# Optimization experiments

Measured on AMD Instinct MI355X. Metric: run time of the kernel, lower is better.

## Reference

```python
import jax, jax.numpy as jnp
import numpy as np

N_HEADS, N_LEVELS, N_POINTS, D_MODEL = 8, 3, 12, 64
PARAM_NAMES = ['vp0_w','vp0_b','vp1_w','vp1_b','so0_w','so0_b','so1_w','so1_b','so2_w','so2_b','so3_w','so3_b','aw0_w','aw0_b','aw1_w','aw1_b','aw2_w','aw2_b','aw3_w','aw3_b','op0_w','op0_b','op1_w','op1_b']

def _lrelu(x):
    return jnp.where(x >= 0, x, 0.1 * x)

def _conv(x, w, b):
    y = jax.lax.conv_general_dilated(x, w, (1, 1), 'SAME', dimension_numbers=('NCHW', 'OIHW', 'NCHW'))
    return y + b[None, :, None, None]

def _bilinear(img, px, py):
    # img [B,C,H,W]; px,py [B,Q] absolute pixel coords; zero padding (grid_sample 'zeros')
    B, C, H, W = img.shape
    flat = img.reshape(B, C, H * W)
    x0 = jnp.floor(px); y0 = jnp.floor(py)
    wx1 = px - x0; wy1 = py - y0
    def g(xi, yi, wgt):
        valid = (xi >= 0) & (xi <= W - 1) & (yi >= 0) & (yi <= H - 1)
        xi_c = jnp.clip(xi, 0, W - 1).astype(jnp.int32)
        yi_c = jnp.clip(yi, 0, H - 1).astype(jnp.int32)
        v = jnp.take_along_axis(flat, (yi_c * W + xi_c)[:, None, :], axis=2)
        return v * (wgt * valid)[:, None, :]
    return (g(x0, y0, (1 - wx1) * (1 - wy1)) + g(x0 + 1, y0, wx1 * (1 - wy1))
          + g(x0, y0 + 1, (1 - wx1) * wy1) + g(x0 + 1, y0 + 1, wx1 * wy1))

def _flow_warp(img, flow):
    # img [n,C,h,w]; flow [n,2,h,w] (x,y); matches grid_sample align_corners=True
    n, C, h, w = img.shape
    gy, gx = jnp.meshgrid(jnp.arange(h, dtype=img.dtype), jnp.arange(w, dtype=img.dtype), indexing='ij')
    px = (gx[None] + flow[:, 0]).reshape(n, h * w)
    py = (gy[None] + flow[:, 1]).reshape(n, h * w)
    return _bilinear(img, px, py).reshape(n, C, h, w)

def _forward(x, flow_1, flow_2, flip_flow_1, flip_flow_2, p):
    n, t, c, h, w = x.shape
    hw = h * w; THW = t * hw
    M, L, P, D = N_HEADS, N_LEVELS, N_POINTS, c // N_HEADS
    flow_cn1 = flow_1
    flow_cn2 = flow_1 + _flow_warp(flow_2, flow_1)
    flow_n1c, flow_n1n2 = flip_flow_1, flow_2
    flow_n2n1 = flip_flow_2
    flow_n2c = flip_flow_2 + _flow_warp(flip_flow_1, flip_flow_2)
    warp_cn1 = _flow_warp(x[:, 1], flow_cn1)
    warp_cn2 = _flow_warp(x[:, 2], flow_cn2)
    warp_n1c = _flow_warp(x[:, 0], flow_n1c)
    warp_n1n2 = _flow_warp(x[:, 2], flow_n1n2)
    warp_n2n1 = _flow_warp(x[:, 1], flow_n2n1)
    warp_n2c = _flow_warp(x[:, 0], flow_n2c)
    extra = jnp.concatenate([x[:, 0], warp_cn1, warp_cn2, warp_n1c, warp_n1n2, warp_n2n1, warp_n2c,
                             flow_cn1, flow_cn2, flow_n1c, flow_n1n2, flow_n2n1, flow_n2c], axis=1)
    value = _conv(_lrelu(_conv(x.reshape(n, t * c, h, w), p['vp0_w'], p['vp0_b'])), p['vp1_w'], p['vp1_b'])
    def head(e, pre):
        y = _lrelu(_conv(e, p[pre + '0_w'], p[pre + '0_b']))
        y = _lrelu(_conv(y, p[pre + '1_w'], p[pre + '1_b']))
        y = _lrelu(_conv(y, p[pre + '2_w'], p[pre + '2_b']))
        return _conv(y, p[pre + '3_w'], p[pre + '3_b'])
    so = head(extra, 'so')  # [n, L*M*L*P*2, h, w]
    aw = head(extra, 'aw')  # [n, L*M*L*P*9, h, w]
    so = so.reshape(n, t, -1, hw).transpose(0, 1, 3, 2).reshape(n, THW, M, L, P, 2)
    aw = aw.reshape(n, t, -1, hw).transpose(0, 1, 3, 2).reshape(n, THW, M, L * P * 9)
    aw = jax.nn.softmax(aw, axis=-1).reshape(n, THW, M, L, P * 9)
    # flow-guided offsets: add per-(query-frame, target-level) flow to learned offsets
    off = so.reshape(n, t, hw, M, L, P, 2)
    fz = jnp.zeros_like(flow_cn2)
    def lvl(f0, f1, f2):
        s = jnp.stack([f0, f1, f2], 1)  # [n,3,2,h,w]
        return s.transpose(0, 3, 4, 1, 2).reshape(n, hw, L, 2)[:, None, :, None, :, None, :]
    off = jnp.concatenate([
        off[:, 0:1] + lvl(fz, flow_cn1, flow_cn2),
        off[:, 1:2] + lvl(flow_n1c, fz, flow_n1n2),
        off[:, 2:3] + lvl(flow_n2c, flow_n2n1, fz)], axis=1).reshape(n, THW, M, L, P, 2)
    # 3x3 integer patch around each sampling point
    pi, pj = jnp.meshgrid(jnp.arange(-1, 2), jnp.arange(-1, 2), indexing='ij')
    patch = jnp.stack([pi, pj], -1).reshape(1, 1, 1, 1, 1, 9, 2).astype(off.dtype)
    off = (off[..., None, :] + patch).reshape(n, THW, M, L, P * 9, 2)
    # reference points (valid_ratios are all 1: full masks are zeros)
    ry, rx = jnp.meshgrid((jnp.arange(h) + 0.5) / h, (jnp.arange(w) + 0.5) / w, indexing='ij')
    ref = jnp.stack([rx, ry], -1).reshape(1, hw, 2).astype(off.dtype)
    ref = jnp.tile(ref, (1, t, 1))  # [1, THW, 2]
    norm = jnp.array([w, h], dtype=off.dtype)
    loc = ref[:, :, None, None, None, :] + off / norm  # [n,THW,M,L,P*9,2] normalized
    # multi-scale deformable attention (all L levels share (h,w)); align_corners=False, zeros pad
    P9 = P * 9
    v = value.reshape(n, t, c, hw).transpose(0, 1, 3, 2).reshape(n, THW, M, D)
    vl = v.reshape(n, L, hw, M, D).transpose(0, 3, 1, 4, 2).reshape(n * M * L, D, h, w)
    px = (loc[..., 0] * w - 0.5).transpose(0, 2, 3, 1, 4).reshape(n * M * L, THW * P9)
    py = (loc[..., 1] * h - 0.5).transpose(0, 2, 3, 1, 4).reshape(n * M * L, THW * P9)
    sampled = _bilinear(vl, px, py).reshape(n, M, L, D, THW, P9)
    out = jnp.einsum('nmldqp,nqmlp->nqmd', sampled, aw).reshape(n, THW, c)
    out = out.reshape(n, t, h, w, c).transpose(0, 1, 4, 2, 3).reshape(n, t * c, h, w)
    out = _conv(_lrelu(_conv(out, p['op0_w'], p['op0_b'])), p['op1_w'], p['op1_b'])
    return out.reshape(n, t, c, h, w) + x

def setup_inputs():
    key = jax.random.key(0)
    n, t, c, h, w = 1, 3, 64, 32, 32
    ks = jax.random.split(key, 24)
    d = {}
    d['x'] = jax.random.normal(ks[0], (n, t, c, h, w), jnp.float32)
    for i, name in enumerate(['flow_1', 'flow_2', 'flip_flow_1', 'flip_flow_2']):
        d[name] = jax.random.normal(ks[1 + i], (n, 2, h, w), jnp.float32)
    cin_extra = 7 * c + 12
    specs = [('vp0', t * c, t * c), ('vp1', t * c, t * c),
             ('so0', c, cin_extra), ('so1', c, c), ('so2', c, c), ('so3', N_LEVELS * N_HEADS * N_LEVELS * N_POINTS * 2, c),
             ('aw0', c, cin_extra), ('aw1', c, c), ('aw2', c, c), ('aw3', N_LEVELS * N_HEADS * N_LEVELS * N_POINTS * 9, c),
             ('op0', t * c, t * c), ('op1', t * c, t * c)]
    for i, (name, co, ci) in enumerate(specs):
        kw, kb = jax.random.split(ks[5 + i])
        std = (2.0 / (ci * 9)) ** 0.5
        d[name + '_w'] = jax.random.normal(kw, (co, ci, 3, 3), jnp.float32) * std
        d[name + '_b'] = jax.random.normal(kb, (co,), jnp.float32) * 0.01
    return d

def reference(x, flow_1, flow_2, flip_flow_1, flip_flow_2, vp0_w, vp0_b, vp1_w, vp1_b, so0_w, so0_b, so1_w, so1_b, so2_w, so2_b, so3_w, so3_b, aw0_w, aw0_b, aw1_w, aw1_b, aw2_w, aw2_b, aw3_w, aw3_b, op0_w, op0_b, op1_w, op1_b):
    p = dict(zip(PARAM_NAMES, (vp0_w, vp0_b, vp1_w, vp1_b, so0_w, so0_b, so1_w, so1_b, so2_w, so2_b, so3_w, so3_b, aw0_w, aw0_b, aw1_w, aw1_b, aw2_w, aw2_b, aw3_w, aw3_b, op0_w, op0_b, op1_w, op1_b)))
    return _forward(x, flow_1, flow_2, flip_flow_1, flip_flow_2, p)
```

## Files before the change

### kernel.cpp

```cpp
#include <hip/hip_runtime.h>
#include <math.h>

#define HW 1024

typedef __attribute__((ext_vector_type(8))) short bf16x8;
typedef __attribute__((ext_vector_type(4))) float floatx4;

__device__ __forceinline__ unsigned short f2bf(float f) {
    unsigned u = __float_as_uint(f);
    u += 0x7FFF + ((u >> 16) & 1);
    return (unsigned short)(u >> 16);
}
__device__ __forceinline__ float bf2f(unsigned short u) {
    return __uint_as_float(((unsigned)u) << 16);
}
__device__ __forceinline__ float bflo(unsigned u) { return __uint_as_float(u << 16); }
__device__ __forceinline__ float bfhi(unsigned u) { return __uint_as_float(u & 0xffff0000u); }

__device__ __forceinline__ float bilin32(const float* __restrict__ img, float px, float py) {
    float x0f = floorf(px), y0f = floorf(py);
    float wx = px - x0f, wy = py - y0f;
    bool vx0 = (x0f >= 0.f) && (x0f <= 31.f);
    bool vx1 = (x0f >= -1.f) && (x0f <= 30.f);
    bool vy0 = (y0f >= 0.f) && (y0f <= 31.f);
    bool vy1 = (y0f >= -1.f) && (y0f <= 30.f);
    int ix0 = (int)fminf(fmaxf(x0f, 0.f), 31.f);
    int iy0 = (int)fminf(fmaxf(y0f, 0.f), 31.f);
    int ix1 = (int)fminf(fmaxf(x0f + 1.f, 0.f), 31.f);
    int iy1 = (int)fminf(fmaxf(y0f + 1.f, 0.f), 31.f);
    float w00 = (1.f - wx) * (1.f - wy) * ((vx0 && vy0) ? 1.f : 0.f);
    float w01 = wx * (1.f - wy) * ((vx1 && vy0) ? 1.f : 0.f);
    float w10 = (1.f - wx) * wy * ((vx0 && vy1) ? 1.f : 0.f);
    float w11 = wx * wy * ((vx1 && vy1) ? 1.f : 0.f);
    return w00 * img[iy0 * 32 + ix0] + w01 * img[iy0 * 32 + ix1] +
           w10 * img[iy1 * 32 + ix0] + w11 * img[iy1 * 32 + ix1];
}

__device__ __forceinline__ float2 comp_flow(const float* __restrict__ fa,
                                            const float* __restrict__ fb, int pix) {
    int y = pix >> 5, x = pix & 31;
    float fx = fa[pix], fy = fa[HW + pix];
    float px = (float)x + fx, py = (float)y + fy;
    float2 r;
    r.x = fx + bilin32(fb, px, py);
    r.y = fy + bilin32(fb + HW, px, py);
    return r;
}

struct WD { const float* src; int cout, Cin, nCb, wbase, beg; };
struct PrepP {
    const float *x, *f1, *f2, *ff1, *ff2;
    float *fcn2, *fn2c;
    unsigned short *x_pad, *extra_pad, *wgt;
    WD wd[12];
};

__global__ __launch_bounds__(256) void prep_k(PrepP P) {
    __shared__ float wlds[16 * 288];
    const int b = blockIdx.x, tid = threadIdx.x;
    if (b < 192) {
        int idx = b * 256 + tid;
        int pix = idx / 48, c4 = idx - pix * 48;
        int y = pix >> 5, xx = pix & 31;
        int c0 = c4 * 4;
        ushort4 s;
        s.x = f2bf(P.x[(size_t)(c0 + 0) * HW + pix]);
        s.y = f2bf(P.x[(size_t)(c0 + 1) * HW + pix]);
        s.z = f2bf(P.x[(size_t)(c0 + 2) * HW + pix]);
        s.w = f2bf(P.x[(size_t)(c0 + 3) * HW + pix]);
        *(ushort4*)(&P.x_pad[(size_t)((y + 1) * 34 + xx + 1) * 192 + c0]) = s;
    } else if (b < 672) {
        int idx = (b - 192) * 256 + tid;
        int pix = idx / 120, c4 = idx - pix * 120;
        int y = pix >> 5, xx = pix & 31;
        int c0 = c4 * 4;
        float va[4];
        if (c0 < 64) {
#pragma unroll
            for (int k = 0; k < 4; ++k) va[k] = P.x[(size_t)(c0 + k) * HW + pix];
        } else if (c0 < 448) {
            int grp = (c0 - 64) >> 6;
            int c = (c0 - 64) & 63;
            const float* src; float fx, fy;
            if (grp == 0)      { src = P.x + 64 * HW;  fx = P.f1[pix];  fy = P.f1[HW + pix]; }
            else if (grp == 1) { src = P.x + 128 * HW; float2 r = comp_flow(P.f1, P.f2, pix);  fx = r.x; fy = r.y; }
            else if (grp == 2) { src = P.x;            fx = P.ff1[pix]; fy = P.ff1[HW + pix]; }
            else if (grp == 3) { src = P.x + 128 * HW; fx = P.f2[pix];  fy = P.f2[HW + pix]; }
            else if (grp == 4) { src = P.x + 64 * HW;  fx = P.ff2[pix]; fy = P.ff2[HW + pix]; }
            else               { src = P.x;            float2 r = comp_flow(P.ff2, P.ff1, pix); fx = r.x; fy = r.y; }
            float px = (float)xx + fx, py = (float)y + fy;
            float x0f = floorf(px), y0f = floorf(py);
            float wx = px - x0f, wy = py - y0f;
            bool vx0 = (x0f >= 0.f) && (x0f <= 31.f);
            bool vx1 = (x0f >= -1.f) && (x0f <= 30.f);
            bool vy0 = (y0f >= 0.f) && (y0f <= 31.f);
            bool vy1 = (y0f >= -1.f) && (y0f <= 30.f);
            int ix0 = (int)fminf(fmaxf(x0f, 0.f), 31.f);
            int iy0 = (int)fminf(fmaxf(y0f, 0.f), 31.f);
            int ix1 = (int)fminf(fmaxf(x0f + 1.f, 0.f), 31.f);
            int iy1 = (int)fminf(fmaxf(y0f + 1.f, 0.f), 31.f);
            float w00 = (1.f - wx) * (1.f - wy) * ((vx0 && vy0) ? 1.f : 0.f);
            float w01 = wx * (1.f - wy) * ((vx1 && vy0) ? 1.f : 0.f);
            float w10 = (1.f - wx) * wy * ((vx0 && vy1) ? 1.f : 0.f);
            float w11 = wx * wy * ((vx1 && vy1) ? 1.f : 0.f);
            int p00 = iy0 * 32 + ix0, p01 = iy0 * 32 + ix1;
            int p10 = iy1 * 32 + ix0, p11 = iy1 * 32 + ix1;
            const float* im = src + (size_t)c * HW;
#pragma unroll
            for (int k = 0; k < 4; ++k) {
                va[k] = w00 * im[p00] + w01 * im[p01] + w10 * im[p10] + w11 * im[p11];
                im += HW;
            }
        } else {
#pragma unroll
            for (int k = 0; k < 4; ++k) {
                int ch = c0 + k;
                float v = 0.f;
                if (ch < 460) {
                    int fc = ch - 448;
                    int which = fc >> 1, comp = fc & 1;
                    if (which == 0)      v = P.f1[comp * HW + pix];
                    else if (which == 1) { float2 r = comp_flow(P.f1, P.f2, pix);  v = comp ? r.y : r.x; }
                    else if (which == 2) v = P.ff1[comp * HW + pix];
                    else if (which == 3) v = P.f2[comp * HW + pix];
                    else if (which == 4) v = P.ff2[comp * HW + pix];
                    else                 { float2 r = comp_flow(P.ff2, P.ff1, pix); v = comp ? r.y : r.x; }
                }
                va[k] = v;
            }
        }
        ushort4 s;
        s.x = f2bf(va[0]); s.y = f2bf(va[1]); s.z = f2bf(va[2]); s.w = f2bf(va[3]);
        *(ushort4*)(&P.extra_pad[(size_t)((y + 1) * 34 + xx + 1) * 480 + c0]) = s;
    } else if (b < 688) {
        int idx = (b - 672) * 256 + tid;
        if (idx < 1024) {
            float2 r = comp_flow(P.f1, P.f2, idx);
            P.fcn2[idx] = r.x; P.fcn2[HW + idx] = r.y;
        } else if (idx < 2048) {
            int pix = idx - 1024;
            float2 r = comp_flow(P.ff2, P.ff1, pix);
            P.fn2c[pix] = r.x; P.fn2c[HW + pix] = r.y;
        }
    } else if (b < 704) {
        const int chans[9] = {192, 192, 480, 64, 64, 64, 64, 192, 192};
        size_t offs[9]; size_t a = 0;
        for (int i = 0; i < 9; ++i) { offs[i] = a; a += (size_t)1156 * chans[i]; }
        int bb = b - 688;
        for (int item = bb; item < 9 * 132; item += 16) {
            int buf = item / 132, i = item - buf * 132;
            int py, px;
            if (i < 34) { py = 0; px = i; }
            else if (i < 68) { py = 33; px = i - 34; }
            else { int j = i - 68; py = 1 + (j >> 1); px = (j & 1) ? 33 : 0; }
            int C = chans[buf];
            unsigned short* p = P.x_pad + offs[buf] + (size_t)(py * 34 + px) * C;
            for (int c = tid; c < C; c += 256) p[c] = 0;
        }
    } else {
        int blk = b - 704;
        int di = 0;
        while (di < 11 && blk >= P.wd[di + 1].beg) ++di;
        WD w = P.wd[di];
        int local = blk - w.beg;
        int co16 = local / w.nCb, cb = local - co16 * w.nCb;
        int cr0 = co16 * 16, ci0 = cb * 32;
        for (int i = tid; i < 16 * 288; i += 256) {
            int cr = i / 288, o = i - cr * 288;
            int crg = cr0 + cr, ci = ci0 + o / 9;
            float v = (crg < w.cout && ci < w.Cin)
                ? w.src[((size_t)crg * w.Cin + ci0) * 9 + o] : 0.f;
            wlds[i] = v;
        }
        __syncthreads();
        for (int e = tid; e < 9 * 512; e += 256) {
            int t = e >> 9, idx = e & 511;
            int j = idx & 7, lane = idx >> 3, q = lane >> 4, mm = lane & 15;
            P.wgt[((size_t)w.wbase + ((size_t)co16 * 9 + t) * w.nCb + cb) * 512 + idx] =
                f2bf(wlds[mm * 288 + (q * 8 + j) * 9 + t]);
        }
    }
}

struct CDesc {
    const unsigned short* in;
    const unsigned short* wgt;
    const float* bias;
    void* out;
    const float* residual;
    int Cpad, nCb, Cout, mode, cmod, relu, Mblocks;
};
struct CParam { CDesc d[4]; };

template<int PIXROWS, int COBLK>
__global__ __launch_bounds__(256) void conv_mfma_k(CParam P) {
    constexpr int TROWS = PIXROWS + 2;
    constexpr int TC = TROWS * 34 * 4;
    constexpr int ITRIPS = (TC + 255) / 256;
    constexpr int NTY = PIXROWS / 4;
    constexpr int NACC = NTY * 2;
    constexpr int MT = COBLK / 16;
    constexpr int WN = MT * 9 * 64;
    constexpr int WTRIPS = (WN + 255) / 256;
    __shared__ unsigned short blds[TROWS * 34 * 40];
    __shared__ unsigned short wlds[MT * 9 * 512];

    int bx = blockIdx.x;
    int di = 0;
    while (bx >= P.d[di].Mblocks) { bx -= P.d[di].Mblocks; ++di; }
    const CDesc d = P.d[di];

    const int tid = threadIdx.x;
    const int w = tid >> 6, lane = tid & 63;
    const int lq = lane >> 4, ln = lane & 15;
    const int co0 = bx * COBLK;
    const int by = blockIdx.y, y0 = by * PIXROWS;
    const unsigned short* __restrict__ in = d.in;
    const unsigned short* __restrict__ wg = d.wgt;
    const int Cpad = d.Cpad, nCb = d.nCb;

    floatx4 acc[MT][NACC];
#pragma unroll
    for (int mt = 0; mt < MT; ++mt)
#pragma unroll
        for (int nt = 0; nt < NACC; ++nt)
            acc[mt][nt] = (floatx4){0.f, 0.f, 0.f, 0.f};

    bf16x8 ireg[ITRIPS];
    bf16x8 wreg[WTRIPS];

    auto load_regs = [&](int cb) {
        const int ci0 = cb << 5;
#pragma unroll
        for (int k = 0; k < ITRIPS; ++k) {
            int i = tid + k * 256;
            if (i < TC) {
                int r = i / 136, rem = i - r * 136, c = rem >> 2, g = rem & 3;
                ireg[k] = *(const bf16x8*)(in + (size_t)((y0 + r) * 34 + c) * Cpad + ci0 + g * 8);
            }
        }
#pragma unroll
        for (int k = 0; k < WTRIPS; ++k) {
            int i = tid + k * 256;
            if (i < WN) {
                int chunk = i >> 6, l16 = i & 63;
                int mt = chunk / 9, t = chunk - mt * 9;
                wreg[k] = *(const bf16x8*)(wg + ((size_t)(((co0 >> 4) + mt) * 9 + t) * nCb + cb) * 512 + l16 * 8);
            }
        }
    };

    load_regs(0);

    for (int cb = 0; cb < nCb; ++cb) {
        __syncthreads();
#pragma unroll
        for (int k = 0; k < ITRIPS; ++k) {
            int i = tid + k * 256;
            if (i < TC) {
                int r = i / 136, rem = i - r * 136, c = rem >> 2, g = rem & 3;
                *(bf16x8*)(&blds[(r * 34 + c) * 40 + g * 8]) = ireg[k];
            }
        }
#pragma unroll
        for (int k = 0; k < WTRIPS; ++k) {
            int i = tid + k * 256;
            if (i < WN) {
                int chunk = i >> 6, l16 = i & 63;
                *(bf16x8*)(&wlds[chunk * 512 + l16 * 8]) = wreg[k];
            }
        }
        __syncthreads();
        if (cb + 1 < nCb) load_regs(cb + 1);
        for (int t = 0; t < 9; ++t) {
            const int dy = t / 3, dx = t - dy * 3;
            bf16x8 bfr[NACC];
#pragma unroll
            for (int ty = 0; ty < NTY; ++ty)
#pragma unroll
                for (int tx = 0; tx < 2; ++tx) {
                    int yy = w * NTY + ty + dy;
                    int xx = tx * 16 + ln + dx;
                    bfr[ty * 2 + tx] = *(const bf16x8*)(&blds[(yy * 34 + xx) * 40 + lq * 8]);
                }
#pragma unroll
            for (int mt = 0; mt < MT; ++mt) {
                bf16x8 afr = *(const bf16x8*)(&wlds[(mt * 9 + t) * 512 + lane * 8]);
#pragma unroll
                for (int nt = 0; nt < NACC; ++nt)
                    acc[mt][nt] = __builtin_amdgcn_mfma_f32_16x16x32_bf16(afr, bfr[nt], acc[mt][nt], 0, 0, 0);
            }
        }
    }

#pragma unroll
    for (int mt = 0; mt < MT; ++mt) {
        const int co = co0 + mt * 16 + lq * 4;
        if (co >= d.Cout) continue;
        float bv[4];
#pragma unroll
        for (int r = 0; r < 4; ++r) bv[r] = d.bias[co + r];
#pragma unroll
        for (int nt = 0; nt < NACC; ++nt) {
            const int ty = nt >> 1, tx = nt & 1;
            const int pix = by * (PIXROWS * 32) + (w * NTY + ty) * 32 + tx * 16 + ln;
            float v[4];
#pragma unroll
            for (int r = 0; r < 4; ++r) {
                float vv = acc[mt][nt][r] + bv[r];
                if (d.relu) vv = (vv >= 0.f) ? vv : 0.1f * vv;
                v[r] = vv;
            }
            if (d.mode == 0) {
                float* o = (float*)d.out;
#pragma unroll
                for (int r = 0; r < 4; ++r) {
                    float vv = v[r];
                    if (d.residual) vv += d.residual[(size_t)(co + r) * HW + pix];
                    o[(size_t)(co + r) * HW + pix] = vv;
                }
            } else if (d.mode == 1) {
                int fq = co / d.cmod, cc = co - fq * d.cmod;
                *(float4*)((float*)d.out + ((size_t)fq * HW + pix) * d.cmod + cc) =
                    make_float4(v[0], v[1], v[2], v[3]);
            } else if (d.mode == 2) {
                int fq = co / d.cmod, cc = co - fq * d.cmod;
                ushort4 s4;
                s4.x = f2bf(v[0]); s4.y = f2bf(v[1]); s4.z = f2bf(v[2]); s4.w = f2bf(v[3]);
                *(ushort4*)((unsigned short*)d.out + ((size_t)fq * HW + pix) * d.cmod + cc) = s4;
            } else {
                int yy = (pix >> 5) + 1, xx = (pix & 31) + 1;
                ushort4 s4;
                s4.x = f2bf(v[0]); s4.y = f2bf(v[1]); s4.z = f2bf(v[2]); s4.w = f2bf(v[3]);
                *(ushort4*)((unsigned short*)d.out + (size_t)(yy * 34 + xx) * d.cmod + co) = s4;
            }
        }
    }
}

__global__ __launch_bounds__(256) void deform_attn_k(
    const unsigned short* __restrict__ value_b, const float* __restrict__ so_t,
    const unsigned short* __restrict__ aw_t,
    const float* __restrict__ flow_1, const float* __restrict__ flow_2,
    const float* __restrict__ flip_flow_1, const float* __restrict__ flip_flow_2,
    const float* __restrict__ flow_cn2, const float* __restrict__ flow_n2c,
    unsigned short* __restrict__ attn_pad)
{
    __shared__ unsigned short vlds[24576];
    __shared__ unsigned short pwlds[4][432];
    const int tid = threadIdx.x;
    const int wav = tid >> 6, lane = tid & 63;
    const int m = blockIdx.x & 7, qc = blockIdx.x >> 3;

    for (int i = tid; i < 3072; i += 256) {
        int l = i >> 10, p = i & 1023;
        *(bf16x8*)(&vlds[(size_t)i * 8]) =
            *(const bf16x8*)(value_b + ((size_t)((l * 8 + m) * 1024) + p) * 8);
    }
    __syncthreads();

    const int pp = lane & 15, gq = lane >> 4;
    const int gdy = (gq >> 1) * 2 - 1;
    const int gdx = (gq & 1) * 2 - 1;
    const bool selx = (gq & 1);
    const bool sely = (gq >> 1);

    float av[6];
    {
        const unsigned short* awp = aw_t + (size_t)(qc * 32 + wav) * 2592 + m * 324;
#pragma unroll
        for (int it = 0; it < 6; ++it) {
            int j = lane + it * 64;
            av[it] = (j < 324) ? bf2f(awp[j]) : -1e30f;
        }
    }

    for (int r = 0; r < 8; ++r) {
        const int q = qc * 32 + r * 4 + wav;
        const int f = q >> 10, pix = q & 1023;
        const int y = pix >> 5, x = pix & 31;

        const float* sop = so_t + (size_t)q * 576 + m * 72;
        float2 so2r[3];
#pragma unroll
        for (int pt = 0; pt < 3; ++pt) {
            int pi = pt * 16 + pp;
            if (pi < 36) so2r[pt] = *(const float2*)(sop + pi * 2);
            else { so2r[pt].x = 0.f; so2r[pt].y = 0.f; }
        }

        float flx0 = 0.f, fly0 = 0.f, flx1 = 0.f, fly1 = 0.f, flx2 = 0.f, fly2 = 0.f;
        if (f == 0) {
            flx1 = flow_1[pix];      fly1 = flow_1[HW + pix];
            flx2 = flow_cn2[pix];    fly2 = flow_cn2[HW + pix];
        } else if (f == 1) {
            flx0 = flip_flow_1[pix]; fly0 = flip_flow_1[HW + pix];
            flx2 = flow_2[pix];      fly2 = flow_2[HW + pix];
        } else {
            flx0 = flow_n2c[pix];    fly0 = flow_n2c[HW + pix];
            flx1 = flip_flow_2[pix]; fly1 = flip_flow_2[HW + pix];
        }

        float vmax = -1e30f;
#pragma unroll
        for (int it = 0; it < 6; ++it) vmax = fmaxf(vmax, av[it]);
#pragma unroll
        for (int off = 32; off; off >>= 1) vmax = fmaxf(vmax, __shfl_xor(vmax, off));
        float ssum = 0.f;
#pragma unroll
        for (int it = 0; it < 6; ++it) {
            int j = lane + it * 64;
            float e = (j < 324) ? __expf(av[it] - vmax) : 0.f;
            av[it] = e;
            ssum += e;
        }
#pragma unroll
        for (int off = 32; off; off >>= 1) ssum += __shfl_xor(ssum, off);
        const float inv = 1.f / ssum;

#pragma unroll
        for (int it = 0; it < 6; ++it) {
            int j = lane + it * 64;
            if (j < 324) {
                int pi = j / 9, k = j - pi * 9;
                pwlds[wav][pi * 12 + k] = f2bf(av[it] * inv);
            }
        }

        float avn[6];
        if (r < 7) {
            const unsigned short* awn = aw_t + (size_t)(q + 4) * 2592 + m * 324;
#pragma unroll
            for (int it = 0; it < 6; ++it) {
                int j = lane + it * 64;
                avn[it] = (j < 324) ? bf2f(awn[j]) : -1e30f;
            }
        }

        float acc[8];
#pragma unroll
        for (int dd = 0; dd < 8; ++dd) acc[dd] = 0.f;

#pragma unroll
        for (int pt = 0; pt < 3; ++pt) {
            int pi = pt * 16 + pp;
            if (pi < 36) {
                int l = pi / 12;
                float2 so2 = so2r[pt];
                float fx = (l == 0) ? flx0 : (l == 1) ? flx1 : flx2;
                float fy = (l == 0) ? fly0 : (l == 1) ? fly1 : fly2;
                float bxf = (float)x + so2.x + fx;
                float byf = (float)y + so2.y + fy;
                float x0f = floorf(bxf), y0f = floorf(byf);
                float wx = bxf - x0f, wy = byf - y0f;
                float ax = 1.f - wx, ay = 1.f - wy;
                int x0 = (int)fminf(fmaxf(x0f, -2.f), 34.f);
                int y0 = (int)fminf(fmaxf(y0f, -2.f), 34.f);

                const unsigned short* pr = &pwlds[wav][pi * 12];
                uint2 pv0 = *(const uint2*)(pr);
                uint2 pv1 = *(const uint2*)(pr + 4);
                float a0 = bflo(pv0.x), a1 = bfhi(pv0.x), a2 = bflo(pv0.y);
                float a3 = bfhi(pv0.y), a4 = bflo(pv1.x), a5 = bfhi(pv1.x);
                float a6 = bflo(pv1.y), a7 = bfhi(pv1.y), a8 = bf2f(pr[8]);

                float bs0a, bs0b, bs1a, bs1b, bs2a, bs2b;
                {
                    float b0, b1, b2, b3;
                    b0 = a0 * ax; b1 = a0 * wx + a3 * ax; b2 = a3 * wx + a6 * ax; b3 = a6 * wx;
                    bs0a = selx ? b2 : b0; bs0b = selx ? b3 : b1;
                    b0 = a1 * ax; b1 = a1 * wx + a4 * ax; b2 = a4 * wx + a7 * ax; b3 = a7 * wx;
                    bs1a = selx ? b2 : b0; bs1b = selx ? b3 : b1;
                    b0 = a2 * ax; b1 = a2 * wx + a5 * ax; b2 = a5 * wx + a8 * ax; b3 = a8 * wx;
                    bs2a = selx ? b2 : b0; bs2b = selx ? b3 : b1;
                }
                float c00, c01, c10, c11;
                {
                    float c0 = bs0a * ay, c1 = bs0a * wy + bs1a * ay;
                    float c2 = bs1a * wy + bs2a * ay, c3 = bs2a * wy;
                    c00 = sely ? c2 : c0; c10 = sely ? c3 : c1;
                    c0 = bs0b * ay; c1 = bs0b * wy + bs1b * ay;
                    c2 = bs1b * wy + bs2b * ay; c3 = bs2b * wy;
                    c01 = sely ? c2 : c0; c11 = sely ? c3 : c1;
                }
                float cg[2][2] = {{c00, c01}, {c10, c11}};
                const int vbase = l * 1024;
#pragma unroll
                for (int sy = 0; sy < 2; ++sy) {
#pragma unroll
                    for (int sx = 0; sx < 2; ++sx) {
                        int dy = gdy + sy, dx = gdx + sx;
                        float pyf = y0f + (float)dy, pxf = x0f + (float)dx;
                        bool v = (pxf >= 0.f) && (pxf <= 31.f) && (pyf >= 0.f) && (pyf <= 31.f);
                        int px = min(max(x0 + dx, 0), 31);
                        int py = min(max(y0 + dy, 0), 31);
                        float c = cg[sy][sx] * (v ? 1.f : 0.f);
                        uint4 vv = *(const uint4*)(&vlds[(size_t)(vbase + py * 32 + px) * 8]);
                        acc[0] = fmaf(c, bflo(vv.x), acc[0]);
                        acc[1] = fmaf(c, bfhi(vv.x), acc[1]);
                        acc[2] = fmaf(c, bflo(vv.y), acc[2]);
                        acc[3] = fmaf(c, bfhi(vv.y), acc[3]);
                        acc[4] = fmaf(c, bflo(vv.z), acc[4]);
                        acc[5] = fmaf(c, bfhi(vv.z), acc[5]);
                        acc[6] = fmaf(c, bflo(vv.w), acc[6]);
                        acc[7] = fmaf(c, bfhi(vv.w), acc[7]);
                    }
                }
            }
        }

#pragma unroll
        for (int dd = 0; dd < 8; ++dd) {
#pragma unroll
            for (int off = 32; off; off >>= 1) acc[dd] += __shfl_xor(acc[dd], off);
        }
        if (lane == 0) {
            unsigned short* op = attn_pad + (size_t)((y + 1) * 34 + x + 1) * 192 + f * 64 + m * 8;
            ushort4 s0, s1;
            s0.x = f2bf(acc[0]); s0.y = f2bf(acc[1]); s0.z = f2bf(acc[2]); s0.w = f2bf(acc[3]);
            s1.x = f2bf(acc[4]); s1.y = f2bf(acc[5]); s1.z = f2bf(acc[6]); s1.w = f2bf(acc[7]);
            *(ushort4*)(op) = s0;
            *(ushort4*)(op + 4) = s1;
        }
        if (r < 7) {
#pragma unroll
            for (int it = 0; it < 6; ++it) av[it] = avn[it];
        }
    }
}

extern "C" void kernel_launch(void* const* d_in, const int* in_sizes, int n_in,
                              void* d_out, int out_size, void* d_ws, size_t ws_size,
                              hipStream_t stream) {
    const float* x      = (const float*)d_in[0];
    const float* flow_1 = (const float*)d_in[1];
    const float* flow_2 = (const float*)d_in[2];
    const float* flip_1 = (const float*)d_in[3];
    const float* flip_2 = (const float*)d_in[4];
    const float* vp0_w = (const float*)d_in[5];  const float* vp0_b = (const float*)d_in[6];
    const float* vp1_w = (const float*)d_in[7];  const float* vp1_b = (const float*)d_in[8];
    const float* so0_w = (const float*)d_in[9];  const float* so0_b = (const float*)d_in[10];
    const float* so1_w = (const float*)d_in[11]; const float* so1_b = (const float*)d_in[12];
    const float* so2_w = (const float*)d_in[13]; const float* so2_b = (const float*)d_in[14];
    const float* so3_w = (const float*)d_in[15]; const float* so3_b = (const float*)d_in[16];
    const float* aw0_w = (const float*)d_in[17]; const float* aw0_b = (const float*)d_in[18];
    const float* aw1_w = (const float*)d_in[19]; const float* aw1_b = (const float*)d_in[20];
    const float* aw2_w = (const float*)d_in[21]; const float* aw2_b = (const float*)d_in[22];
    const float* aw3_w = (const float*)d_in[23]; const float* aw3_b = (const float*)d_in[24];
    const float* op0_w = (const float*)d_in[25]; const float* op0_b = (const float*)d_in[26];
    const float* op1_w = (const float*)d_in[27]; const float* op1_b = (const float*)d_in[28];
    float* out = (float*)d_out;
    (void)ws_size; (void)in_sizes; (void)n_in; (void)out_size;

    float* fws = (float*)d_ws;
    float* flow_cn2 = fws;
    float* flow_n2c = flow_cn2 + 2048;
    unsigned short* value_b = (unsigned short*)(flow_n2c + 2048);
    float* so_t     = (float*)(value_b + 196608);
    unsigned short* uws = (unsigned short*)(so_t + 1769472);
    unsigned short* x_pad     = uws;
    unsigned short* vp0h      = x_pad + 1156 * 192;
    unsigned short* extra_pad = vp0h + 1156 * 192;
    unsigned short* s1 = extra_pad + 1156 * 480;
    unsigned short* a1 = s1 + 1156 * 64;
    unsigned short* s2 = a1 + 1156 * 64;
    unsigned short* a2 = s2 + 1156 * 64;
    unsigned short* attn_pad = a2 + 1156 * 64;
    unsigned short* op0h     = attn_pad + 1156 * 192;
    unsigned short* aw_t = op0h + 1156 * 192;
    unsigned short* wgt  = aw_t + (size_t)3072 * 2592;

    PrepP pp;
    pp.x = x; pp.f1 = flow_1; pp.f2 = flow_2; pp.ff1 = flip_1; pp.ff2 = flip_2;
    pp.fcn2 = flow_cn2; pp.fn2c = flow_n2c;
    pp.x_pad = x_pad; pp.extra_pad = extra_pad; pp.wgt = wgt;
    pp.wd[0]  = {vp0_w, 192, 192, 6,     0,    0};
    pp.wd[1]  = {vp1_w, 192, 192, 6,   648,   72};
    pp.wd[2]  = {so0_w,  64, 460, 15, 1296,  144};
    pp.wd[3]  = {aw0_w,  64, 460, 15, 1836,  204};
    pp.wd[4]  = {so1_w,  64,  64, 2,  2376,  264};
    pp.wd[5]  = {aw1_w,  64,  64, 2,  2448,  272};
    pp.wd[6]  = {so2_w,  64,  64, 2,  2520,  280};
    pp.wd[7]  = {aw2_w,  64,  64, 2,  2592,  288};
    pp.wd[8]  = {so3_w, 1728, 64, 2,  2664,  296};
    pp.wd[9]  = {aw3_w, 7776, 64, 2,  4608,  512};
    pp.wd[10] = {op0_w, 192, 192, 6, 13392, 1488};
    pp.wd[11] = {op1_w, 192, 192, 6, 14040, 1560};
    prep_k<<<2336, 256, 0, stream>>>(pp);

    const int BIG = 1 << 30;
    CDesc nul = {nullptr, nullptr, nullptr, nullptr, nullptr, 0, 0, 0, 0, 0, 0, BIG};

    {
        CParam cp;
        cp.d[0] = {x_pad,     wgt + (size_t)0 * 512,    vp0_b, vp0h, nullptr, 192, 6,  192, 3, 192, 1, 12};
        cp.d[1] = {extra_pad, wgt + (size_t)1296 * 512, so0_b, s1,   nullptr, 480, 15, 64,  3, 64,  1, 4};
        cp.d[2] = {extra_pad, wgt + (size_t)1836 * 512, aw0_b, a1,   nullptr, 480, 15, 64,  3, 64,  1, 4};
        cp.d[3] = nul;
        conv_mfma_k<4, 16><<<dim3(20, 8), 256, 0, stream>>>(cp);
    }
    {
        CParam cp;
        cp.d[0] = {vp0h, wgt + (size_t)648 * 512,  vp1_b, value_b, nullptr, 192, 6, 192, 2, 8,  0, 12};
        cp.d[1] = {s1,   wgt + (size_t)2376 * 512, so1_b, s2,      nullptr, 64,  2, 64,  3, 64, 1, 4};
        cp.d[2] = {a1,   wgt + (size_t)2448 * 512, aw1_b, a2,      nullptr, 64,  2, 64,  3, 64, 1, 4};
        cp.d[3] = nul;
        conv_mfma_k<4, 16><<<dim3(20, 8), 256, 0, stream>>>(cp);
    }
    {
        CParam cp;
        cp.d[0] = {s2, wgt + (size_t)2520 * 512, so2_b, s1, nullptr, 64, 2, 64, 3, 64, 1, 4};
        cp.d[1] = {a2, wgt + (size_t)2592 * 512, aw2_b, a1, nullptr, 64, 2, 64, 3, 64, 1, 4};
        cp.d[2] = nul; cp.d[3] = nul;
        conv_mfma_k<4, 16><<<dim3(8, 8), 256, 0, stream>>>(cp);
    }
    {
        CParam cp;
        cp.d[0] = {s1, wgt + (size_t)2664 * 512, so3_b, so_t, nullptr, 64, 2, 1728, 1, 576,  0, 27};
        cp.d[1] = {a1, wgt + (size_t)4608 * 512, aw3_b, aw_t, nullptr, 64, 2, 7776, 2, 2592, 0, 122};
        cp.d[2] = nul; cp.d[3] = nul;
        conv_mfma_k<8, 64><<<dim3(149, 4), 256, 0, stream>>>(cp);
    }

    deform_attn_k<<<768, 256, 0, stream>>>(value_b, so_t, aw_t,
                                           flow_1, flow_2, flip_1, flip_2,
                                           flow_cn2, flow_n2c, attn_pad);

    {
        CParam cp;
        cp.d[0] = {attn_pad, wgt + (size_t)13392 * 512, op0_b, op0h, nullptr, 192, 6, 192, 3, 192, 1, 12};
        cp.d[1] = nul; cp.d[2] = nul; cp.d[3] = nul;
        conv_mfma_k<4, 16><<<dim3(12, 8), 256, 0, stream>>>(cp);
    }
    {
        CParam cp;
        cp.d[0] = {op0h, wgt + (size_t)14040 * 512, op1_b, out, x, 192, 6, 192, 0, 0, 0, 12};
        cp.d[1] = nul; cp.d[2] = nul; cp.d[3] = nul;
        conv_mfma_k<4, 16><<<dim3(12, 8), 256, 0, stream>>>(cp);
    }
}
```

Measured before the change: 268.7 us.

## Add dedicated kernel for large-output offset/weight convs with per-block output-channel tiling

Replaces the generic conv_mfma_k launch for the so3/aw3 output convolutions (1728 and 7776 output channels, 64 input channels) with a specialized conv_l4_k. Each block owns 16 output channels and keeps all 9-tap weights for both 32-channel input halves resident in LDS. It walks the 32x32 image in 8-row strips and uses register prefetch of the next input strip to overlap global loads with MFMA work. The intent is to cut repeated weight reloads and improve parallelism (594 blocks) for these weight-heavy convs. The trade-off is reloading input strips per block and a hardcoded layout.

Result: no change. 265.3 us (-1.3%).

```diff
diff --git a/kernel.cpp b/kernel.cpp
--- a/kernel.cpp
+++ b/kernel.cpp
@@ -338,6 +338,120 @@
     }
 }
 
+struct L4Desc {
+    const unsigned short* in;
+    const unsigned short* wgt;
+    const float* bias;
+    void* out;
+    int mode, cmod, Mblocks;
+};
+struct L4Param { L4Desc d[2]; };
+
+__global__ __launch_bounds__(256) void conv_l4_k(L4Param P) {
+    __shared__ unsigned short blds[10 * 34 * 40];
+    __shared__ unsigned short wlds[9 * 2 * 512];
+
+    int bx = blockIdx.x;
+    int di = 0;
+    if (bx >= P.d[0].Mblocks) { bx -= P.d[0].Mblocks; di = 1; }
+    const L4Desc d = P.d[di];
+
+    const int tid = threadIdx.x;
+    const int w = tid >> 6, lane = tid & 63;
+    const int lq = lane >> 4, ln = lane & 15;
+    const int co0 = bx * 16;
+    const unsigned short* __restrict__ in = d.in;
+    const unsigned short* __restrict__ wg = d.wgt;
+
+    bf16x8 wreg[5];
+#pragma unroll
+    for (int k = 0; k < 5; ++k) {
+        int i = tid + k * 256;
+        if (i < 1152) {
+            int chunk = i >> 6, l16 = i & 63;
+            int t = chunk >> 1, cb = chunk & 1;
+            wreg[k] = *(const bf16x8*)(wg + (((size_t)bx * 9 + t) * 2 + cb) * 512 + l16 * 8);
+        }
+    }
+
+    bf16x8 ireg[6];
+    auto load_in = [&](int y0, int cb) {
+        const int ci0 = cb << 5;
+#pragma unroll
+        for (int k = 0; k < 6; ++k) {
+            int i = tid + k * 256;
+            if (i < 1360) {
+                int r = i / 136, rem = i - r * 136, c = rem >> 2, g = rem & 3;
+                ireg[k] = *(const bf16x8*)(in + (size_t)((y0 + r) * 34 + c) * 64 + ci0 + g * 8);
+            }
+        }
+    };
+    load_in(0, 0);
+
+#pragma unroll
+    for (int k = 0; k < 5; ++k) {
+        int i = tid + k * 256;
+        if (i < 1152) *(bf16x8*)(&wlds[(i >> 6) * 512 + (i & 63) * 8]) = wreg[k];
+    }
+
+    floatx4 acc[4];
+#pragma unroll
+    for (int nt = 0; nt < 4; ++nt) acc[nt] = (floatx4){0.f, 0.f, 0.f, 0.f};
+
+    for (int p = 0; p < 8; ++p) {
+        const int y = p >> 1, cb = p & 1;
+        __syncthreads();
+#pragma unroll
+        for (int k = 0; k < 6; ++k) {
+            int i = tid + k * 256;
+            if (i < 1360) {
+                int r = i / 136, rem = i - r * 136, c = rem >> 2, g = rem & 3;
+                *(bf16x8*)(&blds[(r * 34 + c) * 40 + g * 8]) = ireg[k];
+            }
+        }
+        __syncthreads();
+        if (p < 7) { int pn = p + 1; load_in((pn >> 1) * 8, pn & 1); }
+#pragma unroll
+        for (int t = 0; t < 9; ++t) {
+            const int dy = t / 3, dx = t - dy * 3;
+            bf16x8 afr = *(const bf16x8*)(&wlds[(t * 2 + cb) * 512 + lane * 8]);
+#pragma unroll
+            for (int ty = 0; ty < 2; ++ty)
+#pragma unroll
+                for (int tx = 0; tx < 2; ++tx) {
+                    int yy = w * 2 + ty + dy;
+                    int xx = tx * 16 + ln + dx;
+                    bf16x8 bfr = *(const bf16x8*)(&blds[(yy * 34 + xx) * 40 + lq * 8]);
+                    acc[ty * 2 + tx] =
+                        __builtin_amdgcn_mfma_f32_16x16x32_bf16(afr, bfr, acc[ty * 2 + tx], 0, 0, 0);
+                }
+        }
+        if (cb == 1) {
+            const int co = co0 + lq * 4;
+            float bv[4];
+#pragma unroll
+            for (int r2 = 0; r2 < 4; ++r2) bv[r2] = d.bias[co + r2];
+            int fq = co / d.cmod, cc = co - fq * d.cmod;
+#pragma unroll
+            for (int nt = 0; nt < 4; ++nt) {
+                const int ty = nt >> 1, tx = nt & 1;
+                const int pix = y * 256 + (w * 2 + ty) * 32 + tx * 16 + ln;
+                float v0 = acc[nt][0] + bv[0], v1 = acc[nt][1] + bv[1];
+                float v2 = acc[nt][2] + bv[2], v3 = acc[nt][3] + bv[3];
+                if (d.mode == 1) {
+                    *(float4*)((float*)d.out + ((size_t)fq * HW + pix) * d.cmod + cc) =
+                        make_float4(v0, v1, v2, v3);
+                } else {
+                    ushort4 s4;
+                    s4.x = f2bf(v0); s4.y = f2bf(v1); s4.z = f2bf(v2); s4.w = f2bf(v3);
+                    *(ushort4*)((unsigned short*)d.out + ((size_t)fq * HW + pix) * d.cmod + cc) = s4;
+                }
+                acc[nt] = (floatx4){0.f, 0.f, 0.f, 0.f};
+            }
+        }
+    }
+}
+
 __global__ __launch_bounds__(256) void deform_attn_k(
     const unsigned short* __restrict__ value_b, const float* __restrict__ so_t,
     const unsigned short* __restrict__ aw_t,
@@ -615,11 +729,10 @@
         conv_mfma_k<4, 16><<<dim3(8, 8), 256, 0, stream>>>(cp);
     }
     {
-        CParam cp;
-        cp.d[0] = {s1, wgt + (size_t)2664 * 512, so3_b, so_t, nullptr, 64, 2, 1728, 1, 576,  0, 27};
-        cp.d[1] = {a1, wgt + (size_t)4608 * 512, aw3_b, aw_t, nullptr, 64, 2, 7776, 2, 2592, 0, 122};
-        cp.d[2] = nul; cp.d[3] = nul;
-        conv_mfma_k<8, 64><<<dim3(149, 4), 256, 0, stream>>>(cp);
+        L4Param lp;
+        lp.d[0] = {s1, wgt + (size_t)2664 * 512, so3_b, so_t, 1, 576,  108};
+        lp.d[1] = {a1, wgt + (size_t)4608 * 512, aw3_b, aw_t, 2, 2592, 486};
+        conv_l4_k<<<594, 256, 0, stream>>>(lp);
     }
 
     deform_attn_k<<<768, 256, 0, stream>>>(value_b, so_t, aw_t,
```
